# Kernel optimization log

Measured on AMD Instinct MI355X. Metric: run time of the kernel, lower is better.

## Reference

```python
import jax, jax.numpy as jnp
import numpy as np

B, T, I, H = 256, 512, 64, 256


def _lstm_layer(x, Wih, Whh, bih, bhh):
    # x: [B, T, in], Wih: [4H, in], Whh: [4H, H], biases: [4H]
    # PyTorch gate order: i, f, g, o.  c' = f*c + i*g ; h = o*tanh(c')
    Hd = Whh.shape[1]
    xp = jnp.einsum('bti,gi->btg', x, Wih) + bih + bhh  # [B, T, 4H]
    h0 = jnp.zeros((x.shape[0], Hd), x.dtype)
    c0 = jnp.zeros((x.shape[0], Hd), x.dtype)

    def step(carry, xt):
        h, c = carry
        g = xt + h @ Whh.T
        i, f, gg, o = jnp.split(g, 4, axis=-1)
        i = jax.nn.sigmoid(i)
        f = jax.nn.sigmoid(f)
        gg = jnp.tanh(gg)
        o = jax.nn.sigmoid(o)
        c = f * c + i * gg
        h = o * jnp.tanh(c)
        return (h, c), h

    _, hs = jax.lax.scan(step, (h0, c0), jnp.swapaxes(xp, 0, 1))  # [T, B, H]
    return jnp.swapaxes(hs, 0, 1)


def setup_inputs() -> dict:
    key = jax.random.key(0)
    ks = jax.random.split(key, 20)
    s_in = 1.0 / np.sqrt(I)
    s_h = 1.0 / np.sqrt(H)
    d = {
        'x': jax.random.normal(ks[0], (B, T, I), jnp.float32),
        # encoder layer 0: input I -> H
        'enc_Wih0': jax.random.normal(ks[1], (4 * H, I), jnp.float32) * s_in,
        'enc_Whh0': jax.random.normal(ks[2], (4 * H, H), jnp.float32) * s_h,
        'enc_bih0': jnp.zeros((4 * H,), jnp.float32),
        'enc_bhh0': jnp.zeros((4 * H,), jnp.float32),
        # encoder layer 1: H -> H
        'enc_Wih1': jax.random.normal(ks[3], (4 * H, H), jnp.float32) * s_h,
        'enc_Whh1': jax.random.normal(ks[4], (4 * H, H), jnp.float32) * s_h,
        'enc_bih1': jnp.zeros((4 * H,), jnp.float32),
        'enc_bhh1': jnp.zeros((4 * H,), jnp.float32),
        # decoder layer 0: H -> H
        'dec_Wih0': jax.random.normal(ks[5], (4 * H, H), jnp.float32) * s_h,
        'dec_Whh0': jax.random.normal(ks[6], (4 * H, H), jnp.float32) * s_h,
        'dec_bih0': jnp.zeros((4 * H,), jnp.float32),
        'dec_bhh0': jnp.zeros((4 * H,), jnp.float32),
        # decoder layer 1: H -> H
        'dec_Wih1': jax.random.normal(ks[7], (4 * H, H), jnp.float32) * s_h,
        'dec_Whh1': jax.random.normal(ks[8], (4 * H, H), jnp.float32) * s_h,
        'dec_bih1': jnp.zeros((4 * H,), jnp.float32),
        'dec_bhh1': jnp.zeros((4 * H,), jnp.float32),
        # output projection H -> I
        'out_W': jax.random.normal(ks[9], (I, H), jnp.float32) * s_h,
        'out_b': jnp.zeros((I,), jnp.float32),
    }
    return d


def reference(x,
              enc_Wih0, enc_Whh0, enc_bih0, enc_bhh0,
              enc_Wih1, enc_Whh1, enc_bih1, enc_bhh1,
              dec_Wih0, dec_Whh0, dec_bih0, dec_bhh0,
              dec_Wih1, dec_Whh1, dec_bih1, dec_bhh1,
              out_W, out_b):
    # Encoder (2 stacked LSTM layers, inference mode -> no inter-layer dropout)
    h = _lstm_layer(x, enc_Wih0, enc_Whh0, enc_bih0, enc_bhh0)
    encoded = _lstm_layer(h, enc_Wih1, enc_Whh1, enc_bih1, enc_bhh1)
    # Decoder (2 stacked LSTM layers over the encoded sequence)
    h = _lstm_layer(encoded, dec_Wih0, dec_Whh0, dec_bih0, dec_bhh0)
    decoded_hidden = _lstm_layer(h, dec_Wih1, dec_Whh1, dec_bih1, dec_bhh1)
    # Linear projection back to input_size
    reconstruction = jnp.einsum('bth,ih->bti', decoded_hidden, out_W) + out_b
    return reconstruction
```

## Files before the change

### kernel.cpp

```cpp
#include <hip/hip_runtime.h>

typedef unsigned short u16;
typedef unsigned int   u32;
typedef _Float16 f16;
typedef _Float16 half2v __attribute__((ext_vector_type(2)));
typedef _Float16 half8v __attribute__((ext_vector_type(8)));
typedef float float4v __attribute__((ext_vector_type(4)));

#define B_  256
#define T_  512
#define I_  64
#define H_  256
#define G_  1024
#define BT_ (B_*T_)

static __device__ __forceinline__ float fdot2u(u32 a, u32 b, float c) {
#if defined(__has_builtin) && __has_builtin(__builtin_amdgcn_fdot2)
  return __builtin_amdgcn_fdot2(__builtin_bit_cast(half2v, a),
                                __builtin_bit_cast(half2v, b), c, false);
#else
  half2v av = __builtin_bit_cast(half2v, a), bv = __builtin_bit_cast(half2v, b);
  return c + (float)av.x * (float)bv.x + (float)av.y * (float)bv.y;
#endif
}

static __device__ __forceinline__ float sig_(float x) {
  return 1.0f / (1.0f + __expf(-x));
}
static __device__ __forceinline__ float tanh_(float x) {
  float ax = fminf(fabsf(x), 15.0f);
  float e  = __expf(2.0f * ax);
  float t  = (e - 1.0f) / (e + 1.0f);
  return copysignf(t, x);
}


__global__ void cvt_f16(const float* __restrict__ in, u16* __restrict__ out, int n) {
  int i = blockIdx.x * blockDim.x + threadIdx.x;
  if (i < n) out[i] = __builtin_bit_cast(u16, (f16)in[i]);
}

__global__ void split_w(const float* __restrict__ w, u16* __restrict__ hi,
                        u16* __restrict__ lo, int n) {
  int i = blockIdx.x * blockDim.x + threadIdx.x;
  if (i < n) {
    float v = w[i];
    f16 h = (f16)v;
    float r = v - (float)h;
    hi[i] = __builtin_bit_cast(u16, h);
    lo[i] = __builtin_bit_cast(u16, (f16)r);
  }
}

__global__ void bias_sum(const float* __restrict__ a, const float* __restrict__ b,
                         float* __restrict__ o, int n) {
  int i = blockIdx.x * blockDim.x + threadIdx.x;
  if (i < n) o[i] = a[i] + b[i];
}

template<int BN>
__global__ __launch_bounds__(256) void gemm_ws(
    const u16* __restrict__ A, const u16* __restrict__ Bh, const u16* __restrict__ Bl,
    const float* __restrict__ bias, float* __restrict__ C,
    int K, int tcl, int t0, int N)
{
  constexpr int BM = 128, BK = 64, LDT = 72;
  __shared__ u16 As[BM * LDT];
  __shared__ u16 Bhs[BN * LDT];
  __shared__ u16 Bls[BN * LDT];
  const int tid = threadIdx.x, wave = tid >> 6, lane = tid & 63;
  const int m0 = blockIdx.x * BM, n0 = blockIdx.y * BN;
  constexpr int WNT = BN / 32;
  const int wm0 = (wave >> 1) * 64, wn0 = (wave & 1) * (BN / 2);
  const int tcmask = (1 << tcl) - 1;
  float4v acc[4][WNT];
  for (int i = 0; i < 4; i++)
    for (int j = 0; j < WNT; j++) acc[i][j] = (float4v){0.f, 0.f, 0.f, 0.f};
  const int lrow = lane & 15, lk = (lane >> 4) * 8;

  for (int k0 = 0; k0 < K; k0 += BK) {
    __syncthreads();
#pragma unroll
    for (int i = 0; i < 4; i++) {
      int idx = tid + i * 256, row = idx >> 3, u = idx & 7;
      int m = m0 + row;
      int rg = (m >> tcl) * T_ + t0 + (m & tcmask);
      *(uint4*)(As + row * LDT + u * 8) =
          *(const uint4*)(A + (size_t)rg * K + k0 + u * 8);
    }
#pragma unroll
    for (int i = 0; i < WNT; i++) {
      int idx = tid + i * 256, row = idx >> 3, u = idx & 7;
      size_t go = (size_t)(n0 + row) * K + k0 + u * 8;
      *(uint4*)(Bhs + row * LDT + u * 8) = *(const uint4*)(Bh + go);
      *(uint4*)(Bls + row * LDT + u * 8) = *(const uint4*)(Bl + go);
    }
    __syncthreads();
#pragma unroll
    for (int ks = 0; ks < 2; ++ks) {
      int col = ks * 32 + lk;
      half8v af[4];
#pragma unroll
      for (int mt = 0; mt < 4; mt++)
        af[mt] = *(const half8v*)(const void*)(As + (wm0 + mt * 16 + lrow) * LDT + col);
#pragma unroll
      for (int nt = 0; nt < WNT; nt++) {
        half8v bhv = *(const half8v*)(const void*)(Bhs + (wn0 + nt * 16 + lrow) * LDT + col);
        half8v blv = *(const half8v*)(const void*)(Bls + (wn0 + nt * 16 + lrow) * LDT + col);
#pragma unroll
        for (int mt = 0; mt < 4; mt++) {
          acc[mt][nt] = __builtin_amdgcn_mfma_f32_16x16x32_f16(af[mt], bhv, acc[mt][nt], 0, 0, 0);
          acc[mt][nt] = __builtin_amdgcn_mfma_f32_16x16x32_f16(af[mt], blv, acc[mt][nt], 0, 0, 0);
        }
      }
    }
  }
  const int crow = (lane >> 4) * 4, ccol = lane & 15;
#pragma unroll
  for (int nt = 0; nt < WNT; nt++) {
    int n = n0 + wn0 + nt * 16 + ccol;
    float bv = bias[n];
#pragma unroll
    for (int mt = 0; mt < 4; mt++) {
#pragma unroll
      for (int r = 0; r < 4; r++) {
        int m = m0 + wm0 + mt * 16 + crow + r;
        C[(size_t)m * N + n] = acc[mt][nt][r] + bv;
      }
    }
  }
}

__global__ __launch_bounds__(512, 1) void lstm_scan(
    const u16* __restrict__ whh, const float* __restrict__ xp,
    u16* __restrict__ hout, float* __restrict__ cst, u16* __restrict__ hst,
    int Tc, int t0)
{
  __shared__ u16 wt[1024 * 72];
  __shared__ u32 h2s[2][128];
  const int tid = threadIdx.x, b = blockIdx.x;
  const int m = tid >> 1;
  const int rA = m + (tid & 1) * 512;
  const int rB = rA + 256;

  uint4 w0q[24], w1q[24];
  const uint4* g0 = (const uint4*)(whh + (size_t)rA * 256);
  const uint4* g1 = (const uint4*)(whh + (size_t)rB * 256);
#pragma unroll
  for (int i = 0; i < 24; i++) { w0q[i] = g0[i]; w1q[i] = g1[i]; }
#pragma unroll
  for (int i = 0; i < 8; i++) {
    *((uint4*)(wt + (size_t)rA * 72) + i) = g0[24 + i];
    *((uint4*)(wt + (size_t)rB * 72) + i) = g1[24 + i];
  }

  float cc = 0.f;
  if (t0 == 0) {
    if (tid < 128) h2s[0][tid] = 0u;
  } else {
    if (!(tid & 1)) cc = cst[(size_t)b * 256 + m];
    if (tid < 128) h2s[0][tid] = ((const u32*)hst)[(size_t)b * 128 + tid];
  }
  __syncthreads();

  const float* xpb = xp + (size_t)b * Tc * 1024;
  float xn0 = xpb[rA], xn1 = xpb[rB];
  u16* houtb = hout + (size_t)b * T_ * 256 + (size_t)t0 * 256;
  const uint4* wt0 = (const uint4*)(wt + (size_t)rA * 72);
  const uint4* wt1 = (const uint4*)(wt + (size_t)rB * 72);

  for (int tt = 0; tt < Tc; ++tt) {
    const int rp = tt & 1, wp = rp ^ 1;
    float a0 = xn0, a1 = xn1;
    if (tt + 1 < Tc) {
      xn0 = xpb[(size_t)(tt + 1) * 1024 + rA];
      xn1 = xpb[(size_t)(tt + 1) * 1024 + rB];
    }
    const uint4* hq = (const uint4*)h2s[rp];
#pragma unroll
    for (int kc = 0; kc < 24; ++kc) {
      uint4 hv = hq[kc];
      uint4 w0 = w0q[kc], w1 = w1q[kc];
      a0 = fdot2u(w0.x, hv.x, a0); a0 = fdot2u(w0.y, hv.y, a0);
      a0 = fdot2u(w0.z, hv.z, a0); a0 = fdot2u(w0.w, hv.w, a0);
      a1 = fdot2u(w1.x, hv.x, a1); a1 = fdot2u(w1.y, hv.y, a1);
      a1 = fdot2u(w1.z, hv.z, a1); a1 = fdot2u(w1.w, hv.w, a1);
    }
#pragma unroll
    for (int kc = 0; kc < 8; ++kc) {
      uint4 hv = hq[24 + kc];
      uint4 w0 = wt0[kc], w1 = wt1[kc];
      a0 = fdot2u(w0.x, hv.x, a0); a0 = fdot2u(w0.y, hv.y, a0);
      a0 = fdot2u(w0.z, hv.z, a0); a0 = fdot2u(w0.w, hv.w, a0);
      a1 = fdot2u(w1.x, hv.x, a1); a1 = fdot2u(w1.y, hv.y, a1);
      a1 = fdot2u(w1.z, hv.z, a1); a1 = fdot2u(w1.w, hv.w, a1);
    }
    float o0 = __shfl_xor(a0, 1);
    float o1 = __shfl_xor(a1, 1);
    if (!(tid & 1)) {
      float iv = sig_(a0), fv = sig_(a1), gv = tanh_(o0), ov = sig_(o1);
      cc = fv * cc + iv * gv;
      float hv = ov * tanh_(cc);
      u16 hb = __builtin_bit_cast(u16, (f16)hv);
      ((u16*)h2s[wp])[m] = hb;
      houtb[(size_t)tt * 256 + m] = hb;
    }
    __syncthreads();
  }
  if (!(tid & 1)) cst[(size_t)b * 256 + m] = cc;
  if (tid < 128) ((u32*)hst)[(size_t)b * 128 + tid] = h2s[Tc & 1][tid];
}


extern "C" void kernel_launch(void* const* d_in, const int* in_sizes, int n_in,
                              void* d_out, int out_size, void* d_ws, size_t ws_size,
                              hipStream_t stream)
{
  const float* x      = (const float*)d_in[0];
  const float* Wih[4] = {(const float*)d_in[1], (const float*)d_in[5],
                         (const float*)d_in[9], (const float*)d_in[13]};
  const float* Whh[4] = {(const float*)d_in[2], (const float*)d_in[6],
                         (const float*)d_in[10], (const float*)d_in[14]};
  const float* bi[4]  = {(const float*)d_in[3], (const float*)d_in[7],
                         (const float*)d_in[11], (const float*)d_in[15]};
  const float* bh[4]  = {(const float*)d_in[4], (const float*)d_in[8],
                         (const float*)d_in[12], (const float*)d_in[16]};
  const float* outW   = (const float*)d_in[17];
  const float* outb   = (const float*)d_in[18];

  char* ws = (char*)d_ws;
  size_t off = 0;
  auto alc = [&](size_t bytes) -> char* {
    char* p = ws + off;
    off = (off + bytes + 255) & ~(size_t)255;
    return p;
  };

  u16* xf  = (u16*)alc((size_t)BT_ * I_ * 2);
  u16* hb0 = (u16*)alc((size_t)BT_ * H_ * 2);
  u16* hb1 = (u16*)alc((size_t)BT_ * H_ * 2);
  int wihn[4] = {G_ * I_, G_ * H_, G_ * H_, G_ * H_};
  u16 *wihH[4], *wihL[4], *whhH[4];
  float* bsum[4];
  for (int l = 0; l < 4; l++) {
    wihH[l] = (u16*)alc((size_t)wihn[l] * 2);
    wihL[l] = (u16*)alc((size_t)wihn[l] * 2);
    whhH[l] = (u16*)alc((size_t)G_ * H_ * 2);
    bsum[l] = (float*)alc((size_t)G_ * 4);
  }
  u16* owH = (u16*)alc((size_t)I_ * H_ * 2);
  u16* owL = (u16*)alc((size_t)I_ * H_ * 2);
  float* cst = (float*)alc((size_t)B_ * H_ * 4);
  u16*   hst = (u16*)alc((size_t)B_ * H_ * 2);

  int Tc = T_;
  while (Tc > 16 && off + (size_t)B_ * Tc * G_ * 4 + 4096 > ws_size) Tc >>= 1;
  float* xpb = (float*)alc((size_t)B_ * Tc * G_ * 4);
  int tcl = 0;
  while ((1 << tcl) < Tc) tcl++;

  {
    int n = BT_ * I_;
    cvt_f16<<<dim3((n + 255) / 256), dim3(256), 0, stream>>>(x, xf, n);
  }
  for (int l = 0; l < 4; l++) {
    split_w<<<dim3((wihn[l] + 255) / 256), dim3(256), 0, stream>>>(Wih[l], wihH[l], wihL[l], wihn[l]);
    cvt_f16<<<dim3((G_ * H_ + 255) / 256), dim3(256), 0, stream>>>(Whh[l], whhH[l], G_ * H_);
    bias_sum<<<dim3(4), dim3(256), 0, stream>>>(bi[l], bh[l], bsum[l], G_);
  }
  split_w<<<dim3((I_ * H_ + 255) / 256), dim3(256), 0, stream>>>(outW, owH, owL, I_ * H_);

  for (int l = 0; l < 4; l++) {
    const u16* Ain = (l == 0) ? xf : ((l == 1) ? hb0 : (l == 2) ? hb1 : hb0);
    u16* Hout = (l & 1) ? hb1 : hb0;
    int K = (l == 0) ? I_ : H_;
    for (int t0 = 0; t0 < T_; t0 += Tc) {
      gemm_ws<128><<<dim3((B_ * Tc) / 128, G_ / 128), dim3(256), 0, stream>>>(
          Ain, wihH[l], wihL[l], bsum[l], xpb, K, tcl, t0, G_);
      lstm_scan<<<dim3(B_), dim3(512), 0, stream>>>(whhH[l], xpb, Hout, cst, hst, Tc, t0);
    }
  }

  gemm_ws<64><<<dim3(BT_ / 128, 1), dim3(256), 0, stream>>>(
      hb1, owH, owL, outb, (float*)d_out, H_, 9, 0, I_);
}
```

Before: 5.688 ms.

## Use one thread per gate row in LSTM scan with gate-interleaved xp layout

```diff
diff --git a/kernel.cpp b/kernel.cpp
--- a/kernel.cpp
+++ b/kernel.cpp
@@ -58,7 +58,7 @@
   if (i < n) o[i] = a[i] + b[i];
 }
 
-template<int BN>
+template<int BN, int PERM>
 __global__ __launch_bounds__(256) void gemm_ws(
     const u16* __restrict__ A, const u16* __restrict__ Bh, const u16* __restrict__ Bl,
     const float* __restrict__ bias, float* __restrict__ C,
@@ -120,85 +120,75 @@
   for (int nt = 0; nt < WNT; nt++) {
     int n = n0 + wn0 + nt * 16 + ccol;
     float bv = bias[n];
+    int ns = PERM ? ((n & 255) * 4 + (n >> 8)) : n;
 #pragma unroll
     for (int mt = 0; mt < 4; mt++) {
 #pragma unroll
       for (int r = 0; r < 4; r++) {
         int m = m0 + wm0 + mt * 16 + crow + r;
-        C[(size_t)m * N + n] = acc[mt][nt][r] + bv;
+        C[(size_t)m * N + ns] = acc[mt][nt][r] + bv;
       }
     }
   }
 }
 
-__global__ __launch_bounds__(512, 1) void lstm_scan(
+__global__ __launch_bounds__(1024, 1) void lstm_scan(
     const u16* __restrict__ whh, const float* __restrict__ xp,
     u16* __restrict__ hout, float* __restrict__ cst, u16* __restrict__ hst,
     int Tc, int t0)
 {
-  __shared__ u16 wt[1024 * 72];
-  __shared__ u32 h2s[2][128];
+  __shared__ __align__(16) u16 wt[1024 * 72];
+  __shared__ __align__(16) u32 h2s[2][128];
   const int tid = threadIdx.x, b = blockIdx.x;
-  const int m = tid >> 1;
-  const int rA = m + (tid & 1) * 512;
-  const int rB = rA + 256;
-
-  uint4 w0q[24], w1q[24];
-  const uint4* g0 = (const uint4*)(whh + (size_t)rA * 256);
-  const uint4* g1 = (const uint4*)(whh + (size_t)rB * 256);
-#pragma unroll
-  for (int i = 0; i < 24; i++) { w0q[i] = g0[i]; w1q[i] = g1[i]; }
-#pragma unroll
-  for (int i = 0; i < 8; i++) {
-    *((uint4*)(wt + (size_t)rA * 72) + i) = g0[24 + i];
-    *((uint4*)(wt + (size_t)rB * 72) + i) = g1[24 + i];
-  }
+  const int q = tid & 3, m = tid >> 2;
+  const int lr = q * 256 + m;
+
+  uint4 wq[24];
+  const uint4* g0 = (const uint4*)(whh + (size_t)lr * 256);
+#pragma unroll
+  for (int i = 0; i < 24; i++) wq[i] = g0[i];
+#pragma unroll
+  for (int i = 0; i < 8; i++)
+    *((uint4*)(wt + (size_t)tid * 72) + i) = g0[24 + i];
 
   float cc = 0.f;
   if (t0 == 0) {
     if (tid < 128) h2s[0][tid] = 0u;
   } else {
-    if (!(tid & 1)) cc = cst[(size_t)b * 256 + m];
+    if (q == 0) cc = cst[(size_t)b * 256 + m];
     if (tid < 128) h2s[0][tid] = ((const u32*)hst)[(size_t)b * 128 + tid];
   }
   __syncthreads();
 
   const float* xpb = xp + (size_t)b * Tc * 1024;
-  float xn0 = xpb[rA], xn1 = xpb[rB];
+  float xn = xpb[tid];
   u16* houtb = hout + (size_t)b * T_ * 256 + (size_t)t0 * 256;
-  const uint4* wt0 = (const uint4*)(wt + (size_t)rA * 72);
-  const uint4* wt1 = (const uint4*)(wt + (size_t)rB * 72);
+  const uint4* wtp = (const uint4*)(wt + (size_t)tid * 72);
 
   for (int tt = 0; tt < Tc; ++tt) {
     const int rp = tt & 1, wp = rp ^ 1;
-    float a0 = xn0, a1 = xn1;
-    if (tt + 1 < Tc) {
-      xn0 = xpb[(size_t)(tt + 1) * 1024 + rA];
-      xn1 = xpb[(size_t)(tt + 1) * 1024 + rB];
-    }
+    float a = xn;
+    if (tt + 1 < Tc) xn = xpb[(size_t)(tt + 1) * 1024 + tid];
     const uint4* hq = (const uint4*)h2s[rp];
 #pragma unroll
     for (int kc = 0; kc < 24; ++kc) {
       uint4 hv = hq[kc];
-      uint4 w0 = w0q[kc], w1 = w1q[kc];
-      a0 = fdot2u(w0.x, hv.x, a0); a0 = fdot2u(w0.y, hv.y, a0);
-      a0 = fdot2u(w0.z, hv.z, a0); a0 = fdot2u(w0.w, hv.w, a0);
-      a1 = fdot2u(w1.x, hv.x, a1); a1 = fdot2u(w1.y, hv.y, a1);
-      a1 = fdot2u(w1.z, hv.z, a1); a1 = fdot2u(w1.w, hv.w, a1);
+      uint4 w0 = wq[kc];
+      a = fdot2u(w0.x, hv.x, a); a = fdot2u(w0.y, hv.y, a);
+      a = fdot2u(w0.z, hv.z, a); a = fdot2u(w0.w, hv.w, a);
     }
 #pragma unroll
     for (int kc = 0; kc < 8; ++kc) {
       uint4 hv = hq[24 + kc];
-      uint4 w0 = wt0[kc], w1 = wt1[kc];
-      a0 = fdot2u(w0.x, hv.x, a0); a0 = fdot2u(w0.y, hv.y, a0);
-      a0 = fdot2u(w0.z, hv.z, a0); a0 = fdot2u(w0.w, hv.w, a0);
-      a1 = fdot2u(w1.x, hv.x, a1); a1 = fdot2u(w1.y, hv.y, a1);
-      a1 = fdot2u(w1.z, hv.z, a1); a1 = fdot2u(w1.w, hv.w, a1);
-    }
-    float o0 = __shfl_xor(a0, 1);
-    float o1 = __shfl_xor(a1, 1);
-    if (!(tid & 1)) {
-      float iv = sig_(a0), fv = sig_(a1), gv = tanh_(o0), ov = sig_(o1);
+      uint4 w0 = wtp[kc];
+      a = fdot2u(w0.x, hv.x, a); a = fdot2u(w0.y, hv.y, a);
+      a = fdot2u(w0.z, hv.z, a); a = fdot2u(w0.w, hv.w, a);
+    }
+    float x1 = __shfl_xor(a, 1);
+    float x2 = __shfl_xor(a, 2);
+    float x3 = __shfl_xor(x1, 2);
+    if (q == 0) {
+      float iv = sig_(a), fv = sig_(x1), gv = tanh_(x2), ov = sig_(x3);
       cc = fv * cc + iv * gv;
       float hv = ov * tanh_(cc);
       u16 hb = __builtin_bit_cast(u16, (f16)hv);
@@ -207,7 +197,7 @@
     }
     __syncthreads();
   }
-  if (!(tid & 1)) cst[(size_t)b * 256 + m] = cc;
+  if (q == 0) cst[(size_t)b * 256 + m] = cc;
   if (tid < 128) ((u32*)hst)[(size_t)b * 128 + tid] = h2s[Tc & 1][tid];
 }
 
@@ -275,12 +265,12 @@
     u16* Hout = (l & 1) ? hb1 : hb0;
     int K = (l == 0) ? I_ : H_;
     for (int t0 = 0; t0 < T_; t0 += Tc) {
-      gemm_ws<128><<<dim3((B_ * Tc) / 128, G_ / 128), dim3(256), 0, stream>>>(
+      gemm_ws<128, 1><<<dim3((B_ * Tc) / 128, G_ / 128), dim3(256), 0, stream>>>(
           Ain, wihH[l], wihL[l], bsum[l], xpb, K, tcl, t0, G_);
-      lstm_scan<<<dim3(B_), dim3(512), 0, stream>>>(whhH[l], xpb, Hout, cst, hst, Tc, t0);
-    }
-  }
-
-  gemm_ws<64><<<dim3(BT_ / 128, 1), dim3(256), 0, stream>>>(
+      lstm_scan<<<dim3(B_), dim3(1024), 0, stream>>>(whhH[l], xpb, Hout, cst, hst, Tc, t0);
+    }
+  }
+
+  gemm_ws<64, 0><<<dim3(BT_ / 128, 1), dim3(256), 0, stream>>>(
       hb1, owH, owL, outb, (float*)d_out, H_, 9, 0, I_);
 }
```

Result: slower. 7.453 ms (+31.0%).
